# Performance work log

Measured on AMD Instinct MI355X. Metric: run time of the kernel, lower is better.

The kernel has to match this reference:

```python
import jax, jax.numpy as jnp
import numpy as np

LN_EPS = 1e-5

def setup_inputs() -> dict:
    key = jax.random.key(0)
    ks = jax.random.split(key, 10)
    L, B, D, C, O = 512, 2, 256, 128, 64
    s_in = 1.0 / np.sqrt(D)
    s_ch = 1.0 / np.sqrt(C)
    return {
        "x": jax.random.normal(ks[0], (L, B, D), dtype=jnp.float32),
        "ln_gamma": jnp.ones((D,), dtype=jnp.float32),
        "ln_beta": jnp.zeros((D,), dtype=jnp.float32),
        "w1": jax.random.uniform(ks[1], (D, C), jnp.float32, -s_in, s_in),
        "b1": jax.random.uniform(ks[2], (C,), jnp.float32, -s_in, s_in),
        "w2": jax.random.uniform(ks[3], (D, C), jnp.float32, -s_in, s_in),
        "b2": jax.random.uniform(ks[4], (C,), jnp.float32, -s_in, s_in),
        "w3": jax.random.uniform(ks[5], (C, O), jnp.float32, -s_ch, s_ch),
        "b3": jax.random.uniform(ks[6], (O,), jnp.float32, -s_ch, s_ch),
        "w4": jax.random.uniform(ks[7], (C, O), jnp.float32, -s_ch, s_ch),
    }

def _layernorm(x, gamma, beta):
    mu = jnp.mean(x, axis=-1, keepdims=True)
    var = jnp.mean(jnp.square(x - mu), axis=-1, keepdims=True)
    return (x - mu) * jax.lax.rsqrt(var + LN_EPS) * gamma + beta

def reference(x, ln_gamma, ln_beta, w1, b1, w2, b2, w3, b3, w4):
    # x: (L, B, D) -> (B, L, D)
    xb = jnp.transpose(x, (1, 0, 2))
    xb = _layernorm(xb, ln_gamma, ln_beta)
    a = xb @ w1 + b1  # (B, L, C)
    b = xb @ w2 + b2  # (B, L, C)
    # (a_l * b_m) @ w3  -> contract channel dim directly into output channels
    mul_term = jnp.einsum('blc,bmc,co->blmo', a, b, w3) + b3
    # (a_l - b_m) @ w4  -> distribute linearity to avoid (B,L,L,C) materialization
    a4 = a @ w4  # (B, L, O)
    b4 = b @ w4  # (B, L, O)
    sub_term = a4[:, :, None, :] - b4[:, None, :, :]
    return mul_term + sub_term  # (B, L, L, O)
```

## Files before the change

kernel.cpp:

```cpp
#include <hip/hip_runtime.h>
#include <hip/hip_bf16.h>

#define LL 512
#define BB 2
#define DD 256
#define CC 128
#define OO 64

#define WT_STRIDE 136

typedef __attribute__((ext_vector_type(8))) short bf16x8;
typedef __attribute__((ext_vector_type(4))) float f32x4;

__device__ __forceinline__ short f2bf(float v) {
    __hip_bfloat16 h = __float2bfloat16(v);
    return *reinterpret_cast<short*>(&h);
}

__device__ __forceinline__ float wave_reduce_sum(float v) {
#pragma unroll
    for (int off = 32; off > 0; off >>= 1)
        v += __shfl_down(v, off, 64);
    return v;
}

__global__ __launch_bounds__(256) void prep_kernel(
    const float* __restrict__ x,
    const float* __restrict__ gamma,
    const float* __restrict__ beta,
    const float* __restrict__ w1, const float* __restrict__ b1,
    const float* __restrict__ w2, const float* __restrict__ b2,
    const float* __restrict__ w4, const float* __restrict__ b3,
    float* __restrict__ a_ws, __hip_bfloat16* __restrict__ bact,
    float* __restrict__ a4b3_ws, float* __restrict__ b4_ws)
{
    const int blk = blockIdx.x;
    const int b = blk >> 9;
    const int l = blk & (LL - 1);
    const int t = threadIdx.x;

    __shared__ float ylds[DD];
    __shared__ float ab[2 * CC];
    __shared__ float red[8];

    float xv = x[(l * BB + b) * DD + t];
    float s = wave_reduce_sum(xv);
    if ((t & 63) == 0) red[t >> 6] = s;
    __syncthreads();
    float mu = (red[0] + red[1] + red[2] + red[3]) * (1.0f / DD);
    float xc = xv - mu;
    float s2 = wave_reduce_sum(xc * xc);
    if ((t & 63) == 0) red[4 + (t >> 6)] = s2;
    __syncthreads();
    float var = (red[4] + red[5] + red[6] + red[7]) * (1.0f / DD);
    float y = xc * rsqrtf(var + 1e-5f) * gamma[t] + beta[t];
    ylds[t] = y;
    __syncthreads();

    {
        const int c = t & (CC - 1);
        const float* w = (t < CC) ? w1 : w2;
        float acc = (t < CC) ? b1[c] : b2[c];
#pragma unroll 16
        for (int d = 0; d < DD; ++d)
            acc = fmaf(ylds[d], w[d * CC + c], acc);
        ab[t] = acc;
        if (t < CC) {
            a_ws[(b * LL + l) * CC + c] = acc;
        } else {
            bact[(b * LL + l) * CC + c] = __float2bfloat16(acc);
        }
    }
    __syncthreads();

    if (t < 2 * OO) {
        const int o = t & (OO - 1);
        const float* src = (t < OO) ? ab : (ab + CC);
        float acc = (t < OO) ? b3[o] : 0.0f;
#pragma unroll 16
        for (int c = 0; c < CC; ++c)
            acc = fmaf(src[c], w4[c * OO + o], acc);
        float* dst = (t < OO) ? a4b3_ws : b4_ws;
        dst[(b * LL + l) * OO + o] = acc;
    }
}

__global__ __launch_bounds__(256, 3) void main_kernel(
    const float* __restrict__ a_ws, const __hip_bfloat16* __restrict__ bact,
    const float* __restrict__ a4b3_ws, const float* __restrict__ b4_ws,
    const float* __restrict__ w3,
    float* __restrict__ out)
{
    const int bid = blockIdx.x;
    const int mh = bid & 1;
    const int l  = (bid >> 1) & (LL - 1);
    const int b  = bid >> 10;
    const int t  = threadIdx.x;
    const int wave = t >> 6;
    const int lane = t & 63;
    const int ln = lane & 15;
    const int q  = lane >> 4;

    __shared__ short Wt[OO * WT_STRIDE];

    const float* arow = a_ws + (b * LL + l) * CC;
    const float4* w3v4 = (const float4*)w3;
#pragma unroll
    for (int i4 = t; i4 < CC * OO / 4; i4 += 256) {
        const int c = i4 >> 4;
        const int o = (i4 & 15) * 4;
        const float ac = arow[c];
        const float4 wv = w3v4[i4];
        Wt[(o + 0) * WT_STRIDE + c] = f2bf(ac * wv.x);
        Wt[(o + 1) * WT_STRIDE + c] = f2bf(ac * wv.y);
        Wt[(o + 2) * WT_STRIDE + c] = f2bf(ac * wv.z);
        Wt[(o + 3) * WT_STRIDE + c] = f2bf(ac * wv.w);
    }
    __syncthreads();

    const int mbase = mh * 256 + wave * 64;

    const short* abase = (const short*)bact + ((size_t)(b * LL + mbase + ln)) * CC + q * 8;
    const short* wbase = &Wt[ln * WT_STRIDE + q * 8];

    f32x4 acc[4][4];
#pragma unroll
    for (int mt = 0; mt < 4; ++mt)
#pragma unroll
        for (int ot = 0; ot < 4; ++ot)
            acc[mt][ot] = (f32x4){0.f, 0.f, 0.f, 0.f};

#pragma unroll
    for (int ks = 0; ks < 4; ++ks) {
        bf16x8 af[4], bfr[4];
#pragma unroll
        for (int mt = 0; mt < 4; ++mt)
            af[mt] = *(const bf16x8*)(abase + mt * (16 * CC) + ks * 32);
#pragma unroll
        for (int ot = 0; ot < 4; ++ot)
            bfr[ot] = *(const bf16x8*)(wbase + ot * (16 * WT_STRIDE) + ks * 32);
#pragma unroll
        for (int mt = 0; mt < 4; ++mt)
#pragma unroll
            for (int ot = 0; ot < 4; ++ot)
                acc[mt][ot] = __builtin_amdgcn_mfma_f32_16x16x32_bf16(
                    af[mt], bfr[ot], acc[mt][ot], 0, 0, 0);
    }

    float a4v[4];
    const float* a4p = a4b3_ws + (b * LL + l) * OO;
#pragma unroll
    for (int ot = 0; ot < 4; ++ot)
        a4v[ot] = a4p[ot * 16 + ln];

#pragma unroll
    for (int mt = 0; mt < 4; ++mt) {
        const int mrow = mbase + mt * 16 + q * 4;
        const float* b4p = b4_ws + ((size_t)(b * LL + mrow)) * OO + ln;
        float* outp = out + (((size_t)(b * LL + l)) * LL + mrow) * OO + ln;
#pragma unroll
        for (int ot = 0; ot < 4; ++ot) {
#pragma unroll
            for (int r = 0; r < 4; ++r) {
                outp[r * OO + ot * 16] = acc[mt][ot][r] + a4v[ot] - b4p[r * OO + ot * 16];
            }
        }
    }
}

extern "C" void kernel_launch(void* const* d_in, const int* in_sizes, int n_in,
                              void* d_out, int out_size, void* d_ws, size_t ws_size,
                              hipStream_t stream) {
    const float* x     = (const float*)d_in[0];
    const float* gamma = (const float*)d_in[1];
    const float* beta  = (const float*)d_in[2];
    const float* w1    = (const float*)d_in[3];
    const float* b1    = (const float*)d_in[4];
    const float* w2    = (const float*)d_in[5];
    const float* b2    = (const float*)d_in[6];
    const float* w3    = (const float*)d_in[7];
    const float* b3    = (const float*)d_in[8];
    const float* w4    = (const float*)d_in[9];
    float* out = (float*)d_out;

    char* ws = (char*)d_ws;
    float* a_ws            = (float*)ws;
    __hip_bfloat16* bact   = (__hip_bfloat16*)(ws + 512*1024);
    float* a4b3_ws         = (float*)(ws + 768*1024);
    float* b4_ws           = (float*)(ws + 1024*1024);

    prep_kernel<<<BB * LL, 256, 0, stream>>>(x, gamma, beta, w1, b1, w2, b2,
                                             w4, b3, a_ws, bact, a4b3_ws, b4_ws);
    main_kernel<<<BB * LL * 2, 256, 0, stream>>>(a_ws, bact, a4b3_ws, b4_ws,
                                                 w3, out);
}
```

Before: 187.6 us.

## Fold w4 subtraction into MFMA weight operand and drop LDS staging

Rewrites the output as b_m·(a_l⊙w3 − w4) + a4b3, so the b4 term is absorbed into the matrix product and the epilogue no longer reads b4. The prep kernel now transposes w3 and w4 into the workspace. The main kernel builds B fragments directly in registers from those transposed weights instead of staging them in LDS behind a barrier. Each wave redundantly recomputes the fragments from cached global loads, and the w4 contribution now goes through bf16 rounding.

```diff
diff --git a/kernel.cpp b/kernel.cpp
--- a/kernel.cpp
+++ b/kernel.cpp
@@ -6,8 +6,6 @@
 #define DD 256
 #define CC 128
 #define OO 64
-
-#define WT_STRIDE 136
 
 typedef __attribute__((ext_vector_type(8))) short bf16x8;
 typedef __attribute__((ext_vector_type(4))) float f32x4;
@@ -31,8 +29,10 @@
     const float* __restrict__ w1, const float* __restrict__ b1,
     const float* __restrict__ w2, const float* __restrict__ b2,
     const float* __restrict__ w4, const float* __restrict__ b3,
+    const float* __restrict__ w3,
     float* __restrict__ a_ws, __hip_bfloat16* __restrict__ bact,
-    float* __restrict__ a4b3_ws, float* __restrict__ b4_ws)
+    float* __restrict__ a4b3_ws,
+    float* __restrict__ w3t_ws, float* __restrict__ w4t_ws)
 {
     const int blk = blockIdx.x;
     const int b = blk >> 9;
@@ -40,8 +40,20 @@
     const int t = threadIdx.x;
 
     __shared__ float ylds[DD];
-    __shared__ float ab[2 * CC];
+    __shared__ float ashare[CC];
     __shared__ float red[8];
+
+    {
+        const int idx = blk * 256 + t;
+        if (idx < 2 * CC * OO) {
+            const float* src = (idx < CC * OO) ? w3 : w4;
+            float* dst = (idx < CC * OO) ? w3t_ws : w4t_ws;
+            const int i = idx & (CC * OO - 1);
+            const int o = i & (OO - 1);
+            const int c = i >> 6;
+            dst[o * CC + c] = src[i];
+        }
+    }
 
     float xv = x[(l * BB + b) * DD + t];
     float s = wave_reduce_sum(xv);
@@ -64,31 +76,28 @@
 #pragma unroll 16
         for (int d = 0; d < DD; ++d)
             acc = fmaf(ylds[d], w[d * CC + c], acc);
-        ab[t] = acc;
         if (t < CC) {
             a_ws[(b * LL + l) * CC + c] = acc;
+            ashare[c] = acc;
         } else {
             bact[(b * LL + l) * CC + c] = __float2bfloat16(acc);
         }
     }
     __syncthreads();
 
-    if (t < 2 * OO) {
-        const int o = t & (OO - 1);
-        const float* src = (t < OO) ? ab : (ab + CC);
-        float acc = (t < OO) ? b3[o] : 0.0f;
+    if (t < OO) {
+        float acc = b3[t];
 #pragma unroll 16
         for (int c = 0; c < CC; ++c)
-            acc = fmaf(src[c], w4[c * OO + o], acc);
-        float* dst = (t < OO) ? a4b3_ws : b4_ws;
-        dst[(b * LL + l) * OO + o] = acc;
+            acc = fmaf(ashare[c], w4[c * OO + t], acc);
+        a4b3_ws[(b * LL + l) * OO + t] = acc;
     }
 }
 
 __global__ __launch_bounds__(256, 3) void main_kernel(
     const float* __restrict__ a_ws, const __hip_bfloat16* __restrict__ bact,
-    const float* __restrict__ a4b3_ws, const float* __restrict__ b4_ws,
-    const float* __restrict__ w3,
+    const float* __restrict__ a4b3_ws,
+    const float* __restrict__ w3t, const float* __restrict__ w4t,
     float* __restrict__ out)
 {
     const int bid = blockIdx.x;
@@ -101,27 +110,16 @@
     const int ln = lane & 15;
     const int q  = lane >> 4;
 
-    __shared__ short Wt[OO * WT_STRIDE];
+    const int mbase = mh * 256 + wave * 64;
 
     const float* arow = a_ws + (b * LL + l) * CC;
-    const float4* w3v4 = (const float4*)w3;
-#pragma unroll
-    for (int i4 = t; i4 < CC * OO / 4; i4 += 256) {
-        const int c = i4 >> 4;
-        const int o = (i4 & 15) * 4;
-        const float ac = arow[c];
-        const float4 wv = w3v4[i4];
-        Wt[(o + 0) * WT_STRIDE + c] = f2bf(ac * wv.x);
-        Wt[(o + 1) * WT_STRIDE + c] = f2bf(ac * wv.y);
-        Wt[(o + 2) * WT_STRIDE + c] = f2bf(ac * wv.z);
-        Wt[(o + 3) * WT_STRIDE + c] = f2bf(ac * wv.w);
-    }
-    __syncthreads();
-
-    const int mbase = mh * 256 + wave * 64;
-
     const short* abase = (const short*)bact + ((size_t)(b * LL + mbase + ln)) * CC + q * 8;
-    const short* wbase = &Wt[ln * WT_STRIDE + q * 8];
+
+    float a4v[4];
+    const float* a4p = a4b3_ws + (b * LL + l) * OO;
+#pragma unroll
+    for (int ot = 0; ot < 4; ++ot)
+        a4v[ot] = a4p[ot * 16 + ln];
 
     f32x4 acc[4][4];
 #pragma unroll
@@ -132,37 +130,52 @@
 
 #pragma unroll
     for (int ks = 0; ks < 4; ++ks) {
-        bf16x8 af[4], bfr[4];
+        const int cb = ks * 32 + q * 8;
+
+        const float4 av0 = *(const float4*)(arow + cb);
+        const float4 av1 = *(const float4*)(arow + cb + 4);
+
+        bf16x8 af[4];
 #pragma unroll
         for (int mt = 0; mt < 4; ++mt)
             af[mt] = *(const bf16x8*)(abase + mt * (16 * CC) + ks * 32);
-#pragma unroll
-        for (int ot = 0; ot < 4; ++ot)
-            bfr[ot] = *(const bf16x8*)(wbase + ot * (16 * WT_STRIDE) + ks * 32);
-#pragma unroll
-        for (int mt = 0; mt < 4; ++mt)
-#pragma unroll
-            for (int ot = 0; ot < 4; ++ot)
+
+#pragma unroll
+        for (int ot = 0; ot < 4; ++ot) {
+            const int o = ot * 16 + ln;
+            const float* w3p = w3t + o * CC + cb;
+            const float* w4p = w4t + o * CC + cb;
+            const float4 x0 = *(const float4*)(w3p);
+            const float4 x1 = *(const float4*)(w3p + 4);
+            const float4 y0 = *(const float4*)(w4p);
+            const float4 y1 = *(const float4*)(w4p + 4);
+
+            bf16x8 bfr;
+            bfr[0] = f2bf(fmaf(av0.x, x0.x, -y0.x));
+            bfr[1] = f2bf(fmaf(av0.y, x0.y, -y0.y));
+            bfr[2] = f2bf(fmaf(av0.z, x0.z, -y0.z));
+            bfr[3] = f2bf(fmaf(av0.w, x0.w, -y0.w));
+            bfr[4] = f2bf(fmaf(av1.x, x1.x, -y1.x));
+            bfr[5] = f2bf(fmaf(av1.y, x1.y, -y1.y));
+            bfr[6] = f2bf(fmaf(av1.z, x1.z, -y1.z));
+            bfr[7] = f2bf(fmaf(av1.w, x1.w, -y1.w));
+
+#pragma unroll
+            for (int mt = 0; mt < 4; ++mt)
                 acc[mt][ot] = __builtin_amdgcn_mfma_f32_16x16x32_bf16(
-                    af[mt], bfr[ot], acc[mt][ot], 0, 0, 0);
-    }
-
-    float a4v[4];
-    const float* a4p = a4b3_ws + (b * LL + l) * OO;
-#pragma unroll
-    for (int ot = 0; ot < 4; ++ot)
-        a4v[ot] = a4p[ot * 16 + ln];
+                    af[mt], bfr, acc[mt][ot], 0, 0, 0);
+        }
+    }
 
 #pragma unroll
     for (int mt = 0; mt < 4; ++mt) {
         const int mrow = mbase + mt * 16 + q * 4;
-        const float* b4p = b4_ws + ((size_t)(b * LL + mrow)) * OO + ln;
         float* outp = out + (((size_t)(b * LL + l)) * LL + mrow) * OO + ln;
 #pragma unroll
         for (int ot = 0; ot < 4; ++ot) {
 #pragma unroll
             for (int r = 0; r < 4; ++r) {
-                outp[r * OO + ot * 16] = acc[mt][ot][r] + a4v[ot] - b4p[r * OO + ot * 16];
+                outp[r * OO + ot * 16] = acc[mt][ot][r] + a4v[ot];
             }
         }
     }
@@ -187,10 +200,12 @@
     float* a_ws            = (float*)ws;
     __hip_bfloat16* bact   = (__hip_bfloat16*)(ws + 512*1024);
     float* a4b3_ws         = (float*)(ws + 768*1024);
-    float* b4_ws           = (float*)(ws + 1024*1024);
+    float* w3t_ws          = (float*)(ws + 1024*1024);
+    float* w4t_ws          = (float*)(ws + 1024*1024 + 32*1024);
 
     prep_kernel<<<BB * LL, 256, 0, stream>>>(x, gamma, beta, w1, b1, w2, b2,
-                                             w4, b3, a_ws, bact, a4b3_ws, b4_ws);
-    main_kernel<<<BB * LL * 2, 256, 0, stream>>>(a_ws, bact, a4b3_ws, b4_ws,
-                                                 w3, out);
-}
+                                             w4, b3, w3,
+                                             a_ws, bact, a4b3_ws, w3t_ws, w4t_ws);
+    main_kernel<<<BB * LL * 2, 256, 0, stream>>>(a_ws, bact, a4b3_ws,
+                                                 w3t_ws, w4t_ws, out);
+}
```

After: 225.9 us. +20.4%, slower.
